# Kernel tuning notes

Measured on AMD Instinct MI355X. Metric: run time of the kernel, lower is better.

The kernel has to match this reference:

```python
import jax, jax.numpy as jnp
import numpy as np

B, C_IN, P, N = 4, 8, 12000, 64
C_PFN = 64          # PFN output channels (hardcoded in source)
H = W = 282         # BEV canvas size (hardcoded)
PILLAR = 0.16       # pillar size in meters
XMIN = YMIN = -22.0 # grid origin (x_edges/y_edges = arange(-22, 22, 0.16))
EPS = 1e-5          # BatchNorm eps (torch default)


def setup_inputs() -> dict:
    key = jax.random.key(0)
    ks = jax.random.split(key, 12)
    # coordinates/features uniform in the grid range so pillars land on the canvas
    sweep = jax.random.uniform(ks[0], (B, C_IN, P, N), jnp.float32, -22.0, 22.0)
    map_in = jax.random.uniform(ks[1], (B, C_IN, P, N), jnp.float32, -22.0, 22.0)
    s = 1.0 / np.sqrt(C_IN)
    w_sweep = jax.random.uniform(ks[2], (C_PFN, C_IN), jnp.float32, -s, s)
    b_sweep = jax.random.uniform(ks[3], (C_PFN,), jnp.float32, -s, s)
    gamma_sweep = 1.0 + 0.1 * jax.random.normal(ks[4], (C_PFN,), jnp.float32)
    beta_sweep = 0.1 * jax.random.normal(ks[5], (C_PFN,), jnp.float32)
    w_map = jax.random.uniform(ks[6], (C_PFN, C_IN), jnp.float32, -s, s)
    b_map = jax.random.uniform(ks[7], (C_PFN,), jnp.float32, -s, s)
    gamma_map = 1.0 + 0.1 * jax.random.normal(ks[8], (C_PFN,), jnp.float32)
    beta_map = 0.1 * jax.random.normal(ks[9], (C_PFN,), jnp.float32)
    sbb = 1.0 / np.sqrt(2 * C_PFN)
    w_bb = jax.random.uniform(ks[10], (C_PFN, 2 * C_PFN), jnp.float32, -sbb, sbb)
    b_bb = jax.random.uniform(ks[11], (C_PFN,), jnp.float32, -sbb, sbb)
    return {"sweep": sweep, "map_in": map_in,
            "w_sweep": w_sweep, "b_sweep": b_sweep,
            "gamma_sweep": gamma_sweep, "beta_sweep": beta_sweep,
            "w_map": w_map, "b_map": b_map,
            "gamma_map": gamma_map, "beta_map": beta_map,
            "w_bb": w_bb, "b_bb": b_bb}


def pfn(x, w, b, gamma, beta):
    # 1x1 conv: [B,8,P,N] -> [B,64,P,N]
    y = jnp.einsum('bcpn,oc->bopn', x, w) + b[None, :, None, None]
    # BatchNorm2d, training-mode batch stats over (B,P,N) per channel
    mean = y.mean(axis=(0, 2, 3), keepdims=True)
    var = y.var(axis=(0, 2, 3), keepdims=True)
    y = (y - mean) * jax.lax.rsqrt(var + EPS)
    y = y * gamma[None, :, None, None] + beta[None, :, None, None]
    y = jax.nn.relu(y)
    return y.max(axis=3)  # max over points -> [B,64,P]


def scatter_to_canvas(inp, feats):
    # inp: [B,8,P,N] (x,y coords at channels 0,1, point 0); feats: [B,64,P]
    x = inp[:, 0, :, 0]  # [B,P]
    y = inp[:, 1, :, 0]
    valid = x != 0  # pillar_list = nonzero(PFN_input[b,0,:,0])
    xg = jnp.clip(jnp.floor((x - XMIN) / PILLAR).astype(jnp.int32), 0, W - 1)
    yg = jnp.clip(jnp.floor((y - YMIN) / PILLAR).astype(jnp.int32), 0, H - 1)
    # route invalid pillars out of bounds so mode='drop' discards them
    xg = jnp.where(valid, xg, W)
    yg = jnp.where(valid, yg, H)
    bidx = jnp.broadcast_to(jnp.arange(B, dtype=jnp.int32)[:, None], (B, P))
    canvas = jnp.zeros((B, H, W, C_PFN), feats.dtype)
    canvas = canvas.at[bidx, yg, xg].set(jnp.swapaxes(feats, 1, 2), mode='drop')
    return jnp.transpose(canvas, (0, 3, 1, 2))  # [B,64,H,W]


def reference(sweep, map_in, w_sweep, b_sweep, gamma_sweep, beta_sweep,
              w_map, b_map, gamma_map, beta_map, w_bb, b_bb):
    sweep_feats = pfn(sweep, w_sweep, b_sweep, gamma_sweep, beta_sweep)
    map_feats = pfn(map_in, w_map, b_map, gamma_map, beta_map)
    sweep_canvas = scatter_to_canvas(sweep, sweep_feats)
    map_canvas = scatter_to_canvas(map_in, map_feats)
    cat = jnp.concatenate([sweep_canvas, map_canvas], axis=1)  # [B,128,H,W]
    # Backbone 1x1 conv (in-channels corrected to 128 to match the data)
    out = jnp.einsum('bchw,oc->bohw', cat, w_bb) + b_bb[None, :, None, None]
    return out
```

## Files before the change

kernel.cpp:

```cpp
#include <hip/hip_runtime.h>
#include <cfloat>
#include <math.h>

namespace {
constexpr int Bn = 4, Cin = 8, Pn = 12000, Nn = 64, Co = 64, Hh = 282, Ww = 282;
constexpr int NPIL  = Bn * Pn;
constexpr int NCELL = Hh * Ww;
constexpr int CHW   = Pn * Nn;
constexpr double CNTD = (double)Bn * Pn * Nn;
constexpr int K1B = 1024;
constexpr int WL_CAP = 48000;
constexpr int APPLY_B = (WL_CAP + 255) / 256;
constexpr int FILL_B = (Bn * Co * NCELL / 4) / 256;

constexpr size_t PAR_OFF  = 0;
constexpr size_t MOM_OFF  = 4608;
constexpr size_t HDR_OFF  = 5376;
constexpr size_t WLS_OFF  = 8192;
constexpr size_t WLM_OFF  = WLS_OFF + (size_t)WL_CAP * 8;
constexpr size_t WIN_OFF  = WLM_OFF + (size_t)WL_CAP * 8;
constexpr size_t FEAT_OFF = WIN_OFF + (size_t)2 * Bn * NCELL * 4;
constexpr size_t PART_OFF = FEAT_OFF;
constexpr size_t WS_NEED  = FEAT_OFF + (size_t)2 * NPIL * 64 * 4;

typedef __attribute__((ext_vector_type(8))) float f32x8_t;
typedef __attribute__((ext_vector_type(2))) float f32x2_t;

__device__ __forceinline__ int cell_of(float xc, float yc) {
  int xg = (int)floorf((xc + 22.0f) * 6.25f);
  int yg = (int)floorf((yc + 22.0f) * 6.25f);
  xg = min(max(xg, 0), Ww - 1);
  yg = min(max(yg, 0), Hh - 1);
  return yg * Ww + xg;
}

__device__ __forceinline__ float firstlane(float v) {
  return __int_as_float(__builtin_amdgcn_readfirstlane(__float_as_int(v)));
}

__device__ __forceinline__ float dpp_xor1(float v) {
  return __int_as_float(__builtin_amdgcn_update_dpp(
      0, __float_as_int(v), 0xB1, 0xF, 0xF, true));
}
__device__ __forceinline__ float dpp_xor2(float v) {
  return __int_as_float(__builtin_amdgcn_update_dpp(
      0, __float_as_int(v), 0x4E, 0xF, 0xF, true));
}
}

__global__ void kdiag(float* __restrict__ out, float v) {
  if (threadIdx.x == 0 && blockIdx.x == 0) out[0] = v;
}

__global__ __launch_bounds__(256) void kinit_fill(
    const float* __restrict__ b_bb, float* __restrict__ out,
    int* __restrict__ winners, int* __restrict__ hdr)
{
  if (blockIdx.x < FILL_B) {
    const int idx = blockIdx.x * 256 + threadIdx.x;
    const int plane = idx / (NCELL / 4);
    const float v = b_bb[plane & 63];
    ((float4*)out)[idx] = make_float4(v, v, v, v);
  } else {
    const int t = (blockIdx.x - FILL_B) * 256 + threadIdx.x;
    if (t < 4) hdr[t] = 0;
    for (int i = t; i < 2 * Bn * NCELL; i += 256 * 256) winners[i] = -1;
  }
}

__global__ __launch_bounds__(256) void k1_mom(
    const float* __restrict__ sweep, const float* __restrict__ map_in,
    float* __restrict__ partOut, int* __restrict__ winners)
{
  __shared__ float red[4][44];
  const int lane = threadIdx.x & 63;
  const int wv   = threadIdx.x >> 6;
  const int bid2 = blockIdx.x & (K1B - 1);
  const int inp  = blockIdx.x / K1B;
  const float* x = inp ? map_in : sweep;
  int* win = winners + inp * Bn * NCELL;
  const int gw   = (bid2 * 256 + (int)threadIdx.x) >> 6;
  const int nw   = (K1B * 256) >> 6;

  float sacc[8];
  float macc[36];
#pragma unroll
  for (int i = 0; i < 8; ++i) sacc[i] = 0.f;
#pragma unroll
  for (int i = 0; i < 36; ++i) macc[i] = 0.f;

  for (int pp = gw; pp < NPIL; pp += nw) {
    const int b = pp / Pn;
    const int p = pp - b * Pn;
    const float* xb = x + (size_t)b * Cin * CHW + (size_t)p * Nn + lane;
    float xv[Cin];
#pragma unroll
    for (int c = 0; c < Cin; ++c) xv[c] = xb[(size_t)c * CHW];
#pragma unroll
    for (int c = 0; c < Cin; ++c) sacc[c] += xv[c];
    {
      int k = 0;
#pragma unroll
      for (int i = 0; i < 8; ++i)
#pragma unroll
        for (int j = i; j < 8; ++j) { macc[k] = fmaf(xv[i], xv[j], macc[k]); ++k; }
    }
    const float xc = firstlane(xv[0]);
    if (xc != 0.0f) {
      const float yc = firstlane(xv[1]);
      if (lane == 0) atomicMax(&win[b * NCELL + cell_of(xc, yc)], p);
    }
  }

#pragma unroll
  for (int k = 0; k < 44; ++k) {
    float v = (k < 8) ? sacc[k] : macc[k - 8];
#pragma unroll
    for (int off = 32; off > 0; off >>= 1) v += __shfl_down(v, off, 64);
    if (lane == 0) red[wv][k] = v;
  }
  __syncthreads();
  if (threadIdx.x < 44) {
    const float s = red[0][threadIdx.x] + red[1][threadIdx.x] +
                    red[2][threadIdx.x] + red[3][threadIdx.x];
    partOut[(size_t)bid2 * 88 + inp * 44 + threadIdx.x] = s;
  }
}

__global__ __launch_bounds__(256) void k1b_reduce(
    const float* __restrict__ part, double* __restrict__ mom)
{
  __shared__ double sd[256];
  const int t = blockIdx.x;
  double s = 0.0;
  for (int blk = threadIdx.x; blk < K1B; blk += 256)
    s += (double)part[(size_t)blk * 88 + t];
  sd[threadIdx.x] = s;
  __syncthreads();
  for (int off = 128; off > 0; off >>= 1) {
    if (threadIdx.x < off) sd[threadIdx.x] += sd[threadIdx.x + off];
    __syncthreads();
  }
  if (threadIdx.x == 0) mom[t] = sd[0];
}

__global__ void k2_params(const double* __restrict__ mom,
    const float* __restrict__ w_s, const float* __restrict__ b_s,
    const float* __restrict__ g_s, const float* __restrict__ be_s,
    const float* __restrict__ w_m, const float* __restrict__ b_m,
    const float* __restrict__ g_m, const float* __restrict__ be_m,
    float* __restrict__ par)
{
  const int t = threadIdx.x;
  if (t >= 128) return;
  const int inp = t >> 6, o = t & 63;
  const double* m = mom + inp * 44;
  const float* w    = (inp ? w_m : w_s) + o * Cin;
  const float bias  = (inp ? b_m : b_s)[o];
  const float gamma = (inp ? g_m : g_s)[o];
  const float beta  = (inp ? be_m : be_s)[o];
  double S[8];
#pragma unroll
  for (int c = 0; c < 8; ++c) S[c] = m[c] / CNTD;
  double mean = (double)bias;
#pragma unroll
  for (int c = 0; c < 8; ++c) mean += (double)w[c] * S[c];
  double var = 0.0;
  int k = 8;
#pragma unroll
  for (int i = 0; i < 8; ++i)
#pragma unroll
    for (int j = i; j < 8; ++j) {
      const double cov = m[k] / CNTD - S[i] * S[j];
      const double ww = (double)w[i] * (double)w[j];
      var += (i == j ? ww : 2.0 * ww) * cov;
      ++k;
    }
  const double a = (double)gamma / sqrt(var + 1e-5);
  float* pr = par + inp * 576;
#pragma unroll
  for (int c = 0; c < 8; ++c) pr[c * 64 + o] = (float)(a * (double)w[c]);
  pr[512 + o] = (float)((double)beta + a * ((double)bias - mean));
}

__global__ __launch_bounds__(256) void k_compact(
    const int* __restrict__ winners, int* __restrict__ hdr,
    int2* __restrict__ wlS, int2* __restrict__ wlM)
{
  __shared__ int cS[4], cM[4];
  __shared__ int baseS, baseM;
  const int t = blockIdx.x * 256 + threadIdx.x;
  const int lane = threadIdx.x & 63;
  const int wv   = threadIdx.x >> 6;
  int ps = -1, pm = -1, outbase = 0, b = 0;
  if (t < Bn * NCELL) {
    b = t / NCELL;
    const int hw = t - b * NCELL;
    outbase = b * Co * NCELL + hw;
    ps = winners[t];
    pm = winners[Bn * NCELL + t];
  }
  const unsigned long long ms = __ballot(ps >= 0);
  const unsigned long long mm = __ballot(pm >= 0);
  if (lane == 0) { cS[wv] = __popcll(ms); cM[wv] = __popcll(mm); }
  __syncthreads();
  if (threadIdx.x == 0) {
    const int c = cS[0] + cS[1] + cS[2] + cS[3];
    baseS = c ? atomicAdd(&hdr[1], c) : 0;
  } else if (threadIdx.x == 64) {
    const int c = cM[0] + cM[1] + cM[2] + cM[3];
    baseM = c ? atomicAdd(&hdr[2], c) : 0;
  }
  __syncthreads();
  const unsigned long long below = (1ull << lane) - 1ull;
  if (ps >= 0) {
    int off = baseS + __popcll(ms & below);
    for (int w2 = 0; w2 < wv; ++w2) off += cS[w2];
    wlS[off] = make_int2(outbase, b * Pn + ps);
  }
  if (pm >= 0) {
    int off = baseM + __popcll(mm & below);
    for (int w2 = 0; w2 < wv; ++w2) off += cM[w2];
    wlM[off] = make_int2(outbase, b * Pn + pm);
  }
}

__global__ __launch_bounds__(256) void k5f_feat(
    const float* __restrict__ sweep, const float* __restrict__ map_in,
    const float* __restrict__ par, const int* __restrict__ winners,
    float* __restrict__ feats)
{
  const int lane = threadIdx.x & 63;
  const int wv   = __builtin_amdgcn_readfirstlane(threadIdx.x >> 6);
  int pp = blockIdx.x * 4 + wv;
  const int inp = (pp >= NPIL) ? 1 : 0;
  pp -= inp * NPIL;
  const float* x   = inp ? map_in : sweep;
  const float* awT = par + inp * 576;
  const float* zbp = awT + 512;
  const int*   win = winners + inp * Bn * NCELL;
  float*       ft  = feats + (size_t)inp * NPIL * 64;

  const int b = pp / Pn;
  const int p = pp - b * Pn;
  const size_t base = (size_t)b * Cin * CHW + (size_t)p * Nn;

  float xv[Cin];
#pragma unroll
  for (int c = 0; c < Cin; ++c) xv[c] = x[base + (size_t)c * CHW + lane];

  const float xc0 = firstlane(xv[0]);
  if (xc0 == 0.0f) return;
  const float yc0 = firstlane(xv[1]);
  const int cell = cell_of(xc0, yc0);
  if (win[b * NCELL + cell] != p) return;

  f32x2_t xd[Cin];
#pragma unroll
  for (int c = 0; c < Cin; ++c) xd[c] = (f32x2_t){xv[c], xv[c]};

  const int l0 = lane & 1, l1 = (lane >> 1) & 1, l2 = (lane >> 2) & 1;
  float res = 0.f;
#pragma unroll
  for (int g = 0; g < 8; ++g) {
    f32x8_t wr0, wr1, wr2, wr3, wr4, wr5, wr6, wr7, zb8;
    asm("s_load_dwordx8 %0, %9, 0x0\n\t"
        "s_load_dwordx8 %1, %9, 0x100\n\t"
        "s_load_dwordx8 %2, %9, 0x200\n\t"
        "s_load_dwordx8 %3, %9, 0x300\n\t"
        "s_load_dwordx8 %4, %9, 0x400\n\t"
        "s_load_dwordx8 %5, %9, 0x500\n\t"
        "s_load_dwordx8 %6, %9, 0x600\n\t"
        "s_load_dwordx8 %7, %9, 0x700\n\t"
        "s_load_dwordx8 %8, %10, 0x0\n\t"
        "s_waitcnt lgkmcnt(0)"
        : "=&s"(wr0), "=&s"(wr1), "=&s"(wr2), "=&s"(wr3), "=&s"(wr4),
          "=&s"(wr5), "=&s"(wr6), "=&s"(wr7), "=&s"(zb8)
        : "s"(awT + g * 8), "s"(zbp + g * 8));

    f32x2_t y0 = {zb8[0], zb8[1]};
    f32x2_t y1 = {zb8[2], zb8[3]};
    f32x2_t y2 = {zb8[4], zb8[5]};
    f32x2_t y3 = {zb8[6], zb8[7]};
#define CH(C, W)                                                              \
    {                                                                         \
      f32x2_t wpa = {W[0], W[1]}, wpb = {W[2], W[3]};                         \
      f32x2_t wpc = {W[4], W[5]}, wpd = {W[6], W[7]};                         \
      asm("v_pk_fma_f32 %0, %1, %2, %0" : "+v"(y0) : "s"(wpa), "v"(xd[C]));   \
      asm("v_pk_fma_f32 %0, %1, %2, %0" : "+v"(y1) : "s"(wpb), "v"(xd[C]));   \
      asm("v_pk_fma_f32 %0, %1, %2, %0" : "+v"(y2) : "s"(wpc), "v"(xd[C]));   \
      asm("v_pk_fma_f32 %0, %1, %2, %0" : "+v"(y3) : "s"(wpd), "v"(xd[C]));   \
    }
    CH(0, wr0) CH(1, wr1) CH(2, wr2) CH(3, wr3)
    CH(4, wr4) CH(5, wr5) CH(6, wr6) CH(7, wr7)
#undef CH
    float z[8] = {y0[0], y0[1], y1[0], y1[1], y2[0], y2[1], y3[0], y3[1]};

    float t0[4];
#pragma unroll
    for (int i = 0; i < 4; ++i) {
      const float send = l0 ? z[2 * i] : z[2 * i + 1];
      const float keep = l0 ? z[2 * i + 1] : z[2 * i];
      t0[i] = fmaxf(keep, dpp_xor1(send));
    }
    float t1[2];
#pragma unroll
    for (int i = 0; i < 2; ++i) {
      const float send = l1 ? t0[2 * i] : t0[2 * i + 1];
      const float keep = l1 ? t0[2 * i + 1] : t0[2 * i];
      t1[i] = fmaxf(keep, dpp_xor2(send));
    }
    {
      const float send = l2 ? t1[0] : t1[1];
      const float keep = l2 ? t1[1] : t1[0];
      float v = fmaxf(keep, __shfl_xor(send, 4, 64));
      v = fmaxf(v, __shfl_xor(v, 8, 64));
      v = fmaxf(v, __shfl_xor(v, 16, 64));
      v = fmaxf(v, __shfl_xor(v, 32, 64));
      if ((lane >> 3) == g) res = v;
    }
  }
  ft[(size_t)pp * 64 + lane] = fmaxf(res, 0.f);
}

template<int WHICH>
__global__ __launch_bounds__(256) void k_apply(
    const int* __restrict__ hdr, const int2* __restrict__ wl,
    const float* __restrict__ feats, const float* __restrict__ w_bb,
    const float* __restrict__ b_bb, float* __restrict__ out)
{
  __shared__ float4 wlds[Co * 16];
  __shared__ float bbb[Co];
  for (int i = threadIdx.x; i < Co * 16; i += 256)
    wlds[i] = ((const float4*)w_bb)[((i >> 4) << 5) + (WHICH ? 16 : 0) + (i & 15)];
  if (threadIdx.x < Co) bbb[threadIdx.x] = b_bb[threadIdx.x];
  __syncthreads();
  const int cnt = hdr[1 + WHICH];
  for (int i = blockIdx.x * blockDim.x + threadIdx.x; i < cnt;
       i += gridDim.x * blockDim.x) {
    const int2 e = wl[i];
    const float4* fp = (const float4*)(feats + (size_t)e.y * 64);
    float4 f[16];
#pragma unroll
    for (int k = 0; k < 16; ++k) f[k] = fp[k];
    float* op = out + e.x;
#pragma unroll 2
    for (int o = 0; o < Co; ++o) {
      float acc = WHICH ? op[(size_t)o * NCELL] : bbb[o];
      const float4* row = &wlds[o * 16];
#pragma unroll
      for (int k = 0; k < 16; ++k) {
        const float4 w4 = row[k];
        acc = fmaf(w4.x, f[k].x, acc); acc = fmaf(w4.y, f[k].y, acc);
        acc = fmaf(w4.z, f[k].z, acc); acc = fmaf(w4.w, f[k].w, acc);
      }
      op[(size_t)o * NCELL] = acc;
    }
  }
}

__global__ void k6_verdict(const int* __restrict__ hdr, float* __restrict__ out)
{
  if (threadIdx.x != 0 || blockIdx.x != 0) return;
  const int n_occ = hdr[1] + hdr[2];
  if (n_occ < 80000 || n_occ > 96000) out[0] = 1.0e7f + (float)n_occ;
}

extern "C" void kernel_launch(void* const* d_in, const int* in_sizes, int n_in,
                              void* d_out, int out_size, void* d_ws, size_t ws_size,
                              hipStream_t stream)
{
  const float* sweep  = (const float*)d_in[0];
  const float* map_in = (const float*)d_in[1];
  const float* w_s  = (const float*)d_in[2];
  const float* b_s  = (const float*)d_in[3];
  const float* g_s  = (const float*)d_in[4];
  const float* be_s = (const float*)d_in[5];
  const float* w_m  = (const float*)d_in[6];
  const float* b_m  = (const float*)d_in[7];
  const float* g_m  = (const float*)d_in[8];
  const float* be_m = (const float*)d_in[9];
  const float* w_bb = (const float*)d_in[10];
  const float* b_bb = (const float*)d_in[11];
  float* out = (float*)d_out;

  const int exp_sz[12] = {24576000, 24576000, 512, 64, 64, 64, 512, 64, 64, 64, 8192, 64};
  int bad_idx = -1;
  if (n_in != 12) bad_idx = 11;
  else for (int i = 0; i < 12; ++i) if (in_sizes[i] != exp_sz[i]) { bad_idx = i; break; }
  if (bad_idx >= 0) {
    kdiag<<<1, 1, 0, stream>>>(out, 9.0e7f + 1.0e5f * (float)bad_idx);
    return;
  }
  if (ws_size < WS_NEED) {
    kdiag<<<1, 1, 0, stream>>>(out, 8.0e7f);
    return;
  }

  char* ws = (char*)d_ws;
  float*  par     = (float*)(ws + PAR_OFF);
  double* mom     = (double*)(ws + MOM_OFF);
  int*    hdr     = (int*)(ws + HDR_OFF);
  int*    winners = (int*)(ws + WIN_OFF);
  float*  feats   = (float*)(ws + FEAT_OFF);
  float*  part    = (float*)(ws + PART_OFF);
  int2*   wlS     = (int2*)(ws + WLS_OFF);
  int2*   wlM     = (int2*)(ws + WLM_OFF);

  kinit_fill<<<FILL_B + 256, 256, 0, stream>>>(b_bb, out, winners, hdr);
  k1_mom<<<2 * K1B, 256, 0, stream>>>(sweep, map_in, part, winners);
  k1b_reduce<<<88, 256, 0, stream>>>(part, mom);
  k2_params<<<1, 128, 0, stream>>>(mom, w_s, b_s, g_s, be_s, w_m, b_m, g_m, be_m, par);
  k_compact<<<(Bn * NCELL + 255) / 256, 256, 0, stream>>>(winners, hdr, wlS, wlM);
  k5f_feat<<<2 * NPIL / 4, 256, 0, stream>>>(sweep, map_in, par, winners, feats);
  k_apply<0><<<APPLY_B, 256, 0, stream>>>(hdr, wlS, feats, w_bb, b_bb, out);
  k_apply<1><<<APPLY_B, 256, 0, stream>>>(hdr, wlM, feats + (size_t)NPIL * 64,
                                          w_bb, b_bb, out);
  k6_verdict<<<1, 1, 0, stream>>>(hdr, out);
}
```

Baseline: 321.6 us.

## Fuse per-pillar PFN max into moment pass, apply BN affine after max

```diff
diff --git a/kernel.cpp b/kernel.cpp
--- a/kernel.cpp
+++ b/kernel.cpp
@@ -14,17 +14,16 @@
 constexpr int FILL_B = (Bn * Co * NCELL / 4) / 256;
 
 constexpr size_t PAR_OFF  = 0;
-constexpr size_t MOM_OFF  = 4608;
-constexpr size_t HDR_OFF  = 5376;
+constexpr size_t MOM_OFF  = 1024;
+constexpr size_t HDR_OFF  = 2048;
 constexpr size_t WLS_OFF  = 8192;
+constexpr size_t PART_OFF = WLS_OFF;
 constexpr size_t WLM_OFF  = WLS_OFF + (size_t)WL_CAP * 8;
 constexpr size_t WIN_OFF  = WLM_OFF + (size_t)WL_CAP * 8;
-constexpr size_t FEAT_OFF = WIN_OFF + (size_t)2 * Bn * NCELL * 4;
-constexpr size_t PART_OFF = FEAT_OFF;
-constexpr size_t WS_NEED  = FEAT_OFF + (size_t)2 * NPIL * 64 * 4;
+constexpr size_t YMAX_OFF = WIN_OFF + (size_t)2 * Bn * NCELL * 4;
+constexpr size_t WS_NEED  = YMAX_OFF + (size_t)2 * NPIL * 64 * 4;
 
 typedef __attribute__((ext_vector_type(8))) float f32x8_t;
-typedef __attribute__((ext_vector_type(2))) float f32x2_t;
 
 __device__ __forceinline__ int cell_of(float xc, float yc) {
   int xg = (int)floorf((xc + 22.0f) * 6.25f);
@@ -63,22 +62,28 @@
     ((float4*)out)[idx] = make_float4(v, v, v, v);
   } else {
     const int t = (blockIdx.x - FILL_B) * 256 + threadIdx.x;
-    if (t < 4) hdr[t] = 0;
+    if (t < 8) hdr[t] = 0;
     for (int i = t; i < 2 * Bn * NCELL; i += 256 * 256) winners[i] = -1;
   }
 }
 
-__global__ __launch_bounds__(256) void k1_mom(
+__global__ __launch_bounds__(256) void k1_momfeat(
     const float* __restrict__ sweep, const float* __restrict__ map_in,
-    float* __restrict__ partOut, int* __restrict__ winners)
+    const float* __restrict__ w_s, const float* __restrict__ b_s,
+    const float* __restrict__ w_m, const float* __restrict__ b_m,
+    float* __restrict__ partOut, int* __restrict__ winners,
+    float* __restrict__ ymax)
 {
   __shared__ float red[4][44];
   const int lane = threadIdx.x & 63;
   const int wv   = threadIdx.x >> 6;
   const int bid2 = blockIdx.x & (K1B - 1);
   const int inp  = blockIdx.x / K1B;
-  const float* x = inp ? map_in : sweep;
-  int* win = winners + inp * Bn * NCELL;
+  const float* x  = inp ? map_in : sweep;
+  const float* w  = inp ? w_m : w_s;
+  const float* bb = inp ? b_m : b_s;
+  int*   win = winners + inp * Bn * NCELL;
+  float* ym  = ymax + (size_t)inp * NPIL * 64;
   const int gw   = (bid2 * 256 + (int)threadIdx.x) >> 6;
   const int nw   = (K1B * 256) >> 6;
 
@@ -88,6 +93,8 @@
   for (int i = 0; i < 8; ++i) sacc[i] = 0.f;
 #pragma unroll
   for (int i = 0; i < 36; ++i) macc[i] = 0.f;
+
+  const int l0 = lane & 1, l1 = (lane >> 1) & 1, l2 = (lane >> 2) & 1;
 
   for (int pp = gw; pp < NPIL; pp += nw) {
     const int b = pp / Pn;
@@ -96,6 +103,7 @@
     float xv[Cin];
 #pragma unroll
     for (int c = 0; c < Cin; ++c) xv[c] = xb[(size_t)c * CHW];
+
 #pragma unroll
     for (int c = 0; c < Cin; ++c) sacc[c] += xv[c];
     {
@@ -105,11 +113,68 @@
 #pragma unroll
         for (int j = i; j < 8; ++j) { macc[k] = fmaf(xv[i], xv[j], macc[k]); ++k; }
     }
+
     const float xc = firstlane(xv[0]);
     if (xc != 0.0f) {
       const float yc = firstlane(xv[1]);
       if (lane == 0) atomicMax(&win[b * NCELL + cell_of(xc, yc)], p);
     }
+
+    float res = 0.f;
+#pragma unroll
+    for (int g = 0; g < 8; ++g) {
+      f32x8_t wr0, wr1, wr2, wr3, wr4, wr5, wr6, wr7, b8;
+      asm("s_load_dwordx8 %0, %9, 0x0\n\t"
+          "s_load_dwordx8 %1, %9, 0x20\n\t"
+          "s_load_dwordx8 %2, %9, 0x40\n\t"
+          "s_load_dwordx8 %3, %9, 0x60\n\t"
+          "s_load_dwordx8 %4, %9, 0x80\n\t"
+          "s_load_dwordx8 %5, %9, 0xA0\n\t"
+          "s_load_dwordx8 %6, %9, 0xC0\n\t"
+          "s_load_dwordx8 %7, %9, 0xE0\n\t"
+          "s_load_dwordx8 %8, %10, 0x0\n\t"
+          "s_waitcnt lgkmcnt(0)"
+          : "=&s"(wr0), "=&s"(wr1), "=&s"(wr2), "=&s"(wr3), "=&s"(wr4),
+            "=&s"(wr5), "=&s"(wr6), "=&s"(wr7), "=&s"(b8)
+          : "s"(w + g * 64), "s"(bb + g * 8));
+
+      float z[8];
+#define PFN_ROW(J, WR)                                                        \
+      {                                                                       \
+        float y = b8[J];                                                      \
+        _Pragma("unroll")                                                     \
+        for (int c = 0; c < Cin; ++c) y = fmaf(WR[c], xv[c], y);              \
+        z[J] = y;                                                             \
+      }
+      PFN_ROW(0, wr0) PFN_ROW(1, wr1) PFN_ROW(2, wr2) PFN_ROW(3, wr3)
+      PFN_ROW(4, wr4) PFN_ROW(5, wr5) PFN_ROW(6, wr6) PFN_ROW(7, wr7)
+#undef PFN_ROW
+
+      float t0[4];
+#pragma unroll
+      for (int i = 0; i < 4; ++i) {
+        const float send = l0 ? z[2 * i] : z[2 * i + 1];
+        const float keep = l0 ? z[2 * i + 1] : z[2 * i];
+        t0[i] = fmaxf(keep, dpp_xor1(send));
+      }
+      float t1[2];
+#pragma unroll
+      for (int i = 0; i < 2; ++i) {
+        const float send = l1 ? t0[2 * i] : t0[2 * i + 1];
+        const float keep = l1 ? t0[2 * i + 1] : t0[2 * i];
+        t1[i] = fmaxf(keep, dpp_xor2(send));
+      }
+      {
+        const float send = l2 ? t1[0] : t1[1];
+        const float keep = l2 ? t1[1] : t1[0];
+        float v = fmaxf(keep, __shfl_xor(send, 4, 64));
+        v = fmaxf(v, __shfl_xor(v, 8, 64));
+        v = fmaxf(v, __shfl_xor(v, 16, 64));
+        v = fmaxf(v, __shfl_xor(v, 32, 64));
+        if ((lane >> 3) == g) res = v;
+      }
+    }
+    ym[(size_t)pp * 64 + lane] = res;
   }
 
 #pragma unroll
@@ -149,7 +214,7 @@
     const float* __restrict__ g_s, const float* __restrict__ be_s,
     const float* __restrict__ w_m, const float* __restrict__ b_m,
     const float* __restrict__ g_m, const float* __restrict__ be_m,
-    float* __restrict__ par)
+    float* __restrict__ par, int* __restrict__ hdr)
 {
   const int t = threadIdx.x;
   if (t >= 128) return;
@@ -177,10 +242,53 @@
       ++k;
     }
   const double a = (double)gamma / sqrt(var + 1e-5);
-  float* pr = par + inp * 576;
-#pragma unroll
-  for (int c = 0; c < 8; ++c) pr[c * 64 + o] = (float)(a * (double)w[c]);
-  pr[512 + o] = (float)((double)beta + a * ((double)bias - mean));
+  const double c = (double)beta - mean * a;
+  const float af = (float)a;
+  par[inp * 128 + o]      = af;
+  par[inp * 128 + 64 + o] = (float)c;
+  if (af < 0.f) atomicOr(&hdr[4 + inp * 2 + (o >> 5)], 1 << (o & 31));
+}
+
+__global__ __launch_bounds__(256) void k_negfix(
+    const float* __restrict__ sweep, const float* __restrict__ map_in,
+    const float* __restrict__ w_s, const float* __restrict__ b_s,
+    const float* __restrict__ w_m, const float* __restrict__ b_m,
+    const int* __restrict__ hdr, float* __restrict__ ymax)
+{
+  const int inp = blockIdx.x & 1;
+  const unsigned m0 = (unsigned)hdr[4 + inp * 2];
+  const unsigned m1 = (unsigned)hdr[5 + inp * 2];
+  if ((m0 | m1) == 0u) return;
+  const float* x  = inp ? map_in : sweep;
+  const float* w  = inp ? w_m : w_s;
+  const float* bb = inp ? b_m : b_s;
+  float* ym = ymax + (size_t)inp * NPIL * 64;
+  const int lane = threadIdx.x & 63;
+  const int wv   = threadIdx.x >> 6;
+  const int gw   = (int)(blockIdx.x >> 1) * 4 + wv;
+  const int nw   = (int)(gridDim.x >> 1) * 4;
+  for (int pp = gw; pp < NPIL; pp += nw) {
+    const int b = pp / Pn;
+    const int p = pp - b * Pn;
+    const size_t base = (size_t)b * Cin * CHW + (size_t)p * Nn;
+    float xv[Cin];
+#pragma unroll
+    for (int c = 0; c < Cin; ++c) xv[c] = x[base + (size_t)c * CHW + lane];
+    for (int half = 0; half < 2; ++half) {
+      unsigned m = half ? m1 : m0;
+      while (m) {
+        const int bit = __ffs(m) - 1;
+        m &= m - 1;
+        const int o = half * 32 + bit;
+        float y = bb[o];
+#pragma unroll
+        for (int c = 0; c < Cin; ++c) y = fmaf(w[o * Cin + c], xv[c], y);
+#pragma unroll
+        for (int s = 1; s < 64; s <<= 1) y = fminf(y, __shfl_xor(y, s, 64));
+        if (lane == 0) ym[(size_t)pp * 64 + o] = y;
+      }
+    }
+  }
 }
 
 __global__ __launch_bounds__(256) void k_compact(
@@ -225,124 +333,39 @@
   }
 }
 
-__global__ __launch_bounds__(256) void k5f_feat(
-    const float* __restrict__ sweep, const float* __restrict__ map_in,
-    const float* __restrict__ par, const int* __restrict__ winners,
-    float* __restrict__ feats)
-{
-  const int lane = threadIdx.x & 63;
-  const int wv   = __builtin_amdgcn_readfirstlane(threadIdx.x >> 6);
-  int pp = blockIdx.x * 4 + wv;
-  const int inp = (pp >= NPIL) ? 1 : 0;
-  pp -= inp * NPIL;
-  const float* x   = inp ? map_in : sweep;
-  const float* awT = par + inp * 576;
-  const float* zbp = awT + 512;
-  const int*   win = winners + inp * Bn * NCELL;
-  float*       ft  = feats + (size_t)inp * NPIL * 64;
-
-  const int b = pp / Pn;
-  const int p = pp - b * Pn;
-  const size_t base = (size_t)b * Cin * CHW + (size_t)p * Nn;
-
-  float xv[Cin];
-#pragma unroll
-  for (int c = 0; c < Cin; ++c) xv[c] = x[base + (size_t)c * CHW + lane];
-
-  const float xc0 = firstlane(xv[0]);
-  if (xc0 == 0.0f) return;
-  const float yc0 = firstlane(xv[1]);
-  const int cell = cell_of(xc0, yc0);
-  if (win[b * NCELL + cell] != p) return;
-
-  f32x2_t xd[Cin];
-#pragma unroll
-  for (int c = 0; c < Cin; ++c) xd[c] = (f32x2_t){xv[c], xv[c]};
-
-  const int l0 = lane & 1, l1 = (lane >> 1) & 1, l2 = (lane >> 2) & 1;
-  float res = 0.f;
-#pragma unroll
-  for (int g = 0; g < 8; ++g) {
-    f32x8_t wr0, wr1, wr2, wr3, wr4, wr5, wr6, wr7, zb8;
-    asm("s_load_dwordx8 %0, %9, 0x0\n\t"
-        "s_load_dwordx8 %1, %9, 0x100\n\t"
-        "s_load_dwordx8 %2, %9, 0x200\n\t"
-        "s_load_dwordx8 %3, %9, 0x300\n\t"
-        "s_load_dwordx8 %4, %9, 0x400\n\t"
-        "s_load_dwordx8 %5, %9, 0x500\n\t"
-        "s_load_dwordx8 %6, %9, 0x600\n\t"
-        "s_load_dwordx8 %7, %9, 0x700\n\t"
-        "s_load_dwordx8 %8, %10, 0x0\n\t"
-        "s_waitcnt lgkmcnt(0)"
-        : "=&s"(wr0), "=&s"(wr1), "=&s"(wr2), "=&s"(wr3), "=&s"(wr4),
-          "=&s"(wr5), "=&s"(wr6), "=&s"(wr7), "=&s"(zb8)
-        : "s"(awT + g * 8), "s"(zbp + g * 8));
-
-    f32x2_t y0 = {zb8[0], zb8[1]};
-    f32x2_t y1 = {zb8[2], zb8[3]};
-    f32x2_t y2 = {zb8[4], zb8[5]};
-    f32x2_t y3 = {zb8[6], zb8[7]};
-#define CH(C, W)                                                              \
-    {                                                                         \
-      f32x2_t wpa = {W[0], W[1]}, wpb = {W[2], W[3]};                         \
-      f32x2_t wpc = {W[4], W[5]}, wpd = {W[6], W[7]};                         \
-      asm("v_pk_fma_f32 %0, %1, %2, %0" : "+v"(y0) : "s"(wpa), "v"(xd[C]));   \
-      asm("v_pk_fma_f32 %0, %1, %2, %0" : "+v"(y1) : "s"(wpb), "v"(xd[C]));   \
-      asm("v_pk_fma_f32 %0, %1, %2, %0" : "+v"(y2) : "s"(wpc), "v"(xd[C]));   \
-      asm("v_pk_fma_f32 %0, %1, %2, %0" : "+v"(y3) : "s"(wpd), "v"(xd[C]));   \
-    }
-    CH(0, wr0) CH(1, wr1) CH(2, wr2) CH(3, wr3)
-    CH(4, wr4) CH(5, wr5) CH(6, wr6) CH(7, wr7)
-#undef CH
-    float z[8] = {y0[0], y0[1], y1[0], y1[1], y2[0], y2[1], y3[0], y3[1]};
-
-    float t0[4];
-#pragma unroll
-    for (int i = 0; i < 4; ++i) {
-      const float send = l0 ? z[2 * i] : z[2 * i + 1];
-      const float keep = l0 ? z[2 * i + 1] : z[2 * i];
-      t0[i] = fmaxf(keep, dpp_xor1(send));
-    }
-    float t1[2];
-#pragma unroll
-    for (int i = 0; i < 2; ++i) {
-      const float send = l1 ? t0[2 * i] : t0[2 * i + 1];
-      const float keep = l1 ? t0[2 * i + 1] : t0[2 * i];
-      t1[i] = fmaxf(keep, dpp_xor2(send));
-    }
-    {
-      const float send = l2 ? t1[0] : t1[1];
-      const float keep = l2 ? t1[1] : t1[0];
-      float v = fmaxf(keep, __shfl_xor(send, 4, 64));
-      v = fmaxf(v, __shfl_xor(v, 8, 64));
-      v = fmaxf(v, __shfl_xor(v, 16, 64));
-      v = fmaxf(v, __shfl_xor(v, 32, 64));
-      if ((lane >> 3) == g) res = v;
-    }
-  }
-  ft[(size_t)pp * 64 + lane] = fmaxf(res, 0.f);
-}
-
 template<int WHICH>
 __global__ __launch_bounds__(256) void k_apply(
     const int* __restrict__ hdr, const int2* __restrict__ wl,
-    const float* __restrict__ feats, const float* __restrict__ w_bb,
-    const float* __restrict__ b_bb, float* __restrict__ out)
+    const float* __restrict__ ymax, const float* __restrict__ par,
+    const float* __restrict__ w_bb, const float* __restrict__ b_bb,
+    float* __restrict__ out)
 {
   __shared__ float4 wlds[Co * 16];
   __shared__ float bbb[Co];
+  __shared__ float av[Co], cv[Co];
   for (int i = threadIdx.x; i < Co * 16; i += 256)
     wlds[i] = ((const float4*)w_bb)[((i >> 4) << 5) + (WHICH ? 16 : 0) + (i & 15)];
-  if (threadIdx.x < Co) bbb[threadIdx.x] = b_bb[threadIdx.x];
+  if (threadIdx.x < Co) {
+    bbb[threadIdx.x] = b_bb[threadIdx.x];
+    av[threadIdx.x]  = par[WHICH * 128 + threadIdx.x];
+    cv[threadIdx.x]  = par[WHICH * 128 + 64 + threadIdx.x];
+  }
   __syncthreads();
+  const float* ybase = ymax + (size_t)WHICH * NPIL * 64;
   const int cnt = hdr[1 + WHICH];
   for (int i = blockIdx.x * blockDim.x + threadIdx.x; i < cnt;
        i += gridDim.x * blockDim.x) {
     const int2 e = wl[i];
-    const float4* fp = (const float4*)(feats + (size_t)e.y * 64);
+    const float4* yp = (const float4*)(ybase + (size_t)e.y * 64);
     float4 f[16];
 #pragma unroll
-    for (int k = 0; k < 16; ++k) f[k] = fp[k];
+    for (int k = 0; k < 16; ++k) {
+      const float4 ymv = yp[k];
+      f[k].x = fmaxf(fmaf(av[4 * k + 0], ymv.x, cv[4 * k + 0]), 0.f);
+      f[k].y = fmaxf(fmaf(av[4 * k + 1], ymv.y, cv[4 * k + 1]), 0.f);
+      f[k].z = fmaxf(fmaf(av[4 * k + 2], ymv.z, cv[4 * k + 2]), 0.f);
+      f[k].w = fmaxf(fmaf(av[4 * k + 3], ymv.w, cv[4 * k + 3]), 0.f);
+    }
     float* op = out + e.x;
 #pragma unroll 2
     for (int o = 0; o < Co; ++o) {
@@ -402,19 +425,20 @@
   double* mom     = (double*)(ws + MOM_OFF);
   int*    hdr     = (int*)(ws + HDR_OFF);
   int*    winners = (int*)(ws + WIN_OFF);
-  float*  feats   = (float*)(ws + FEAT_OFF);
+  float*  ymax    = (float*)(ws + YMAX_OFF);
   float*  part    = (float*)(ws + PART_OFF);
   int2*   wlS     = (int2*)(ws + WLS_OFF);
   int2*   wlM     = (int2*)(ws + WLM_OFF);
 
   kinit_fill<<<FILL_B + 256, 256, 0, stream>>>(b_bb, out, winners, hdr);
-  k1_mom<<<2 * K1B, 256, 0, stream>>>(sweep, map_in, part, winners);
+  k1_momfeat<<<2 * K1B, 256, 0, stream>>>(sweep, map_in, w_s, b_s, w_m, b_m,
+                                          part, winners, ymax);
   k1b_reduce<<<88, 256, 0, stream>>>(part, mom);
-  k2_params<<<1, 128, 0, stream>>>(mom, w_s, b_s, g_s, be_s, w_m, b_m, g_m, be_m, par);
+  k2_params<<<1, 128, 0, stream>>>(mom, w_s, b_s, g_s, be_s, w_m, b_m, g_m, be_m,
+                                   par, hdr);
+  k_negfix<<<1024, 256, 0, stream>>>(sweep, map_in, w_s, b_s, w_m, b_m, hdr, ymax);
   k_compact<<<(Bn * NCELL + 255) / 256, 256, 0, stream>>>(winners, hdr, wlS, wlM);
-  k5f_feat<<<2 * NPIL / 4, 256, 0, stream>>>(sweep, map_in, par, winners, feats);
-  k_apply<0><<<APPLY_B, 256, 0, stream>>>(hdr, wlS, feats, w_bb, b_bb, out);
-  k_apply<1><<<APPLY_B, 256, 0, stream>>>(hdr, wlM, feats + (size_t)NPIL * 64,
-                                          w_bb, b_bb, out);
+  k_apply<0><<<APPLY_B, 256, 0, stream>>>(hdr, wlS, ymax, par, w_bb, b_bb, out);
+  k_apply<1><<<APPLY_B, 256, 0, stream>>>(hdr, wlM, ymax, par, w_bb, b_bb, out);
   k6_verdict<<<1, 1, 0, stream>>>(hdr, out);
 }
```

Result: slower. 329.8 us (+2.6%).
